# Kernel tuning notes

Measured on AMD Instinct MI355X. Metric: run time of the kernel, lower is better.

## Reference

```python
import jax, jax.numpy as jnp
import numpy as np

B, N, D, H, O = 4096, 128, 64, 256, 128  # batch, memory_size, memory_dim, controller_dim, output_size


def setup_inputs() -> dict:
    key = jax.random.key(0)
    ks = jax.random.split(key, 20)
    s = 0.05
    inp = {
        "x": jax.random.normal(ks[0], (B, O), jnp.float32),
        "memory": jax.random.normal(ks[1], (B, N, D), jnp.float32),
        "h": jax.random.normal(ks[2], (B, H), jnp.float32),
        "c": jax.random.normal(ks[3], (B, H), jnp.float32),
        # LSTMCell params (torch layout: gates ordered i, f, g, o; input = x||read_vec of width O+D)
        "W_ih": jax.random.normal(ks[4], (4 * H, O + D), jnp.float32) * s,
        "W_hh": jax.random.normal(ks[5], (4 * H, H), jnp.float32) * s,
        "b_ih": jax.random.normal(ks[6], (4 * H,), jnp.float32) * s,
        "b_hh": jax.random.normal(ks[7], (4 * H,), jnp.float32) * s,
        "W_read": jax.random.normal(ks[8], (N, H), jnp.float32) * s,
        "b_read": jax.random.normal(ks[9], (N,), jnp.float32) * s,
        "W_write": jax.random.normal(ks[10], (N, H), jnp.float32) * s,
        "b_write": jax.random.normal(ks[11], (N,), jnp.float32) * s,
        "W_erase": jax.random.normal(ks[12], (D, H), jnp.float32) * s,
        "b_erase": jax.random.normal(ks[13], (D,), jnp.float32) * s,
        "W_add": jax.random.normal(ks[14], (D, H), jnp.float32) * s,
        "b_add": jax.random.normal(ks[15], (D,), jnp.float32) * s,
        "W_out": jax.random.normal(ks[16], (O, H + D), jnp.float32) * s,
        "b_out": jax.random.normal(ks[17], (O,), jnp.float32) * s,
    }
    return inp


def reference(x, memory, h, c, W_ih, W_hh, b_ih, b_hh, W_read, b_read,
              W_write, b_write, W_erase, b_erase, W_add, b_add, W_out, b_out):
    # read: softmax attention over memory rows, addressed by previous hidden state
    read_w = jax.nn.softmax(h @ W_read.T + b_read, axis=-1)          # [B, N]
    read_vec = jnp.einsum("bn,bnd->bd", read_w, memory)               # [B, D]

    # LSTMCell step (torch gate order: i, f, g, o)
    ctrl_in = jnp.concatenate([x, read_vec], axis=-1)                 # [B, O+D]
    gates = ctrl_in @ W_ih.T + b_ih + h @ W_hh.T + b_hh               # [B, 4H]
    i, f, g, o = jnp.split(gates, 4, axis=-1)
    i, f, o = jax.nn.sigmoid(i), jax.nn.sigmoid(f), jax.nn.sigmoid(o)
    g = jnp.tanh(g)
    c_new = f * c + i * g
    h_new = o * jnp.tanh(c_new)

    # write: outer-product erase/add update
    write_w = jax.nn.softmax(h_new @ W_write.T + b_write, axis=-1)    # [B, N]
    erase = jax.nn.sigmoid(h_new @ W_erase.T + b_erase)               # [B, D]
    add = jnp.tanh(h_new @ W_add.T + b_add)                           # [B, D]
    ww = write_w[:, :, None]                                          # [B, N, 1]
    mem_new = memory * (1.0 - ww * erase[:, None, :]) + ww * add[:, None, :]

    out = jnp.concatenate([h_new, read_vec], axis=-1) @ W_out.T + b_out  # [B, O]
    return (out, mem_new, h_new, c_new)
```

## Files before the change

### kernel.cpp

```cpp
#include <hip/hip_runtime.h>
#include <math.h>


typedef __attribute__((ext_vector_type(8))) short bf16x8;
typedef __attribute__((ext_vector_type(4))) float f32x4;
typedef __attribute__((ext_vector_type(4))) unsigned short us4;

#define MFMA16(a, b, c) __builtin_amdgcn_mfma_f32_16x16x32_bf16(a, b, c, 0, 0, 0)
#define GLL16(gp, lp) __builtin_amdgcn_global_load_lds( \
    (const __attribute__((address_space(1))) void*)(gp), \
    (__attribute__((address_space(3))) void*)(lp), 16, 0, 0)
#define SW(row, s) ((s) ^ ((row) & 3))

__device__ __forceinline__ float sigf(float v) { return 1.f / (1.f + __expf(-v)); }

__device__ __forceinline__ unsigned short f2bf(float f) {
    unsigned u = __builtin_bit_cast(unsigned, f);
    u = (u + 0x7FFFu + ((u >> 16) & 1u)) >> 16;
    return (unsigned short)u;
}

__global__ __launch_bounds__(256) void kA_scores(
    const float* __restrict__ h, const float* __restrict__ Wr,
    const float* __restrict__ br, float* __restrict__ read_w)
{
    __shared__ unsigned short As[16 * 32];
    __shared__ unsigned short Bs[128 * 32];
    __shared__ float sc[16][128];

    int t = threadIdx.x;
    int wid = t >> 6, lane = t & 63;
    int cl = lane & 15, ks = lane >> 4;
    int b0 = blockIdx.x * 16;

    int aOff = cl * 32 + SW(cl, ks) * 8;
    int bOff[4];
#pragma unroll
    for (int f = 0; f < 4; ++f) {
        int br_ = (wid * 4 + f) * 16 + cl;
        bOff[f] = br_ * 32 + SW(br_, ks) * 8;
    }
    f32x4 acc[4] = {};
    for (int kc = 0; kc < 8; ++kc) {
        __syncthreads();
        {
            int row = t >> 4, k0 = (t & 15) * 2;
            float2 hv = *(const float2*)(h + (size_t)(b0 + row) * 256 + kc * 32 + k0);
            unsigned pk = (unsigned)f2bf(hv.x) | ((unsigned)f2bf(hv.y) << 16);
            *(unsigned*)(As + row * 32 + SW(row, k0 >> 3) * 8 + (k0 & 7)) = pk;
        }
        {
            int row = t >> 1, k0 = (t & 1) * 16;
            const float4* wp = (const float4*)(Wr + (size_t)row * 256 + kc * 32 + k0);
            float4 w0 = wp[0], w1 = wp[1], w2 = wp[2], w3 = wp[3];
            us4 p0 = { f2bf(w0.x), f2bf(w0.y), f2bf(w0.z), f2bf(w0.w) };
            us4 p1 = { f2bf(w1.x), f2bf(w1.y), f2bf(w1.z), f2bf(w1.w) };
            us4 p2 = { f2bf(w2.x), f2bf(w2.y), f2bf(w2.z), f2bf(w2.w) };
            us4 p3 = { f2bf(w3.x), f2bf(w3.y), f2bf(w3.z), f2bf(w3.w) };
            int g0 = k0 >> 3;
            unsigned short* basep = Bs + row * 32;
            *(us4*)(basep + SW(row, g0) * 8)         = p0;
            *(us4*)(basep + SW(row, g0) * 8 + 4)     = p1;
            *(us4*)(basep + SW(row, g0 + 1) * 8)     = p2;
            *(us4*)(basep + SW(row, g0 + 1) * 8 + 4) = p3;
        }
        __syncthreads();
        if (wid < 2) {
            bf16x8 a = *(const bf16x8*)(As + aOff);
#pragma unroll
            for (int f = 0; f < 4; ++f)
                acc[f] = MFMA16(a, *(const bf16x8*)(Bs + bOff[f]), acc[f]);
        }
    }
    if (wid < 2) {
#pragma unroll
        for (int f = 0; f < 4; ++f)
#pragma unroll
            for (int r = 0; r < 4; ++r)
                sc[ks * 4 + r][(wid * 4 + f) * 16 + cl] = acc[f][r];
    }
    __syncthreads();
    {
        int row = t >> 4, l = t & 15;
        float v[8];
#pragma unroll
        for (int j = 0; j < 8; ++j) v[j] = sc[row][l + 16 * j] + br[l + 16 * j];
        float m = v[0];
#pragma unroll
        for (int j = 1; j < 8; ++j) m = fmaxf(m, v[j]);
#pragma unroll
        for (int mk = 8; mk >= 1; mk >>= 1) m = fmaxf(m, __shfl_xor(m, mk));
        float s = 0.f;
#pragma unroll
        for (int j = 0; j < 8; ++j) { v[j] = __expf(v[j] - m); s += v[j]; }
#pragma unroll
        for (int mk = 8; mk >= 1; mk >>= 1) s += __shfl_xor(s, mk);
        float inv = 1.f / s;
#pragma unroll
        for (int j = 0; j < 8; ++j)
            read_w[(size_t)(b0 + row) * 128 + l + 16 * j] = v[j] * inv;
    }
}

__global__ __launch_bounds__(256) void k2_stream_pack(
    const float* __restrict__ mem, const float* __restrict__ read_w,
    const float* __restrict__ x, const float* __restrict__ h,
    const float* __restrict__ Wih, const float* __restrict__ Whh,
    const float* __restrict__ bih, const float* __restrict__ bhh,
    const float* __restrict__ Ww, const float* __restrict__ We,
    const float* __restrict__ Wa, const float* __restrict__ bw,
    const float* __restrict__ be, const float* __restrict__ ba,
    const float* __restrict__ Wo,
    unsigned short* __restrict__ Wg, unsigned short* __restrict__ Wh_b,
    unsigned short* __restrict__ Wo_b, float* __restrict__ bsum,
    float* __restrict__ bh_b, unsigned short* __restrict__ Ag,
    unsigned short* __restrict__ Aout)
{
    __shared__ float part[16][68];
    int t = threadIdx.x;
    int b = blockIdx.x;
    unsigned idx = b * 256 + t;

    if (idx < 458752) {
        int r = idx / 448, cc = idx - r * 448;
        float v = (cc < 192) ? Wih[(size_t)r * 192 + cc] : Whh[(size_t)r * 256 + (cc - 192)];
        Wg[idx] = f2bf(v);
    }
    if (idx < 65536) {
        int r = idx >> 8, cc = idx & 255;
        float v = (r < 128) ? Ww[(size_t)r * 256 + cc]
                : (r < 192) ? We[(size_t)(r - 128) * 256 + cc]
                            : Wa[(size_t)(r - 192) * 256 + cc];
        Wh_b[idx] = f2bf(v);
    }
    if (idx < 40960) Wo_b[idx] = f2bf(Wo[idx]);
    if (idx < 1024)  bsum[idx] = bih[idx] + bhh[idx];
    if (idx < 256)
        bh_b[idx] = (idx < 128) ? bw[idx] : (idx < 192 ? be[idx - 128] : ba[idx - 192]);

    if (t < 96) {
        int j = t;
        float4 v = (j < 32) ? ((const float4*)(x + (size_t)b * 128))[j]
                            : ((const float4*)(h + (size_t)b * 256))[j - 32];
        us4 o = { f2bf(v.x), f2bf(v.y), f2bf(v.z), f2bf(v.w) };
        int col = (j < 32) ? j * 4 : 192 + (j - 32) * 4;
        *(us4*)(Ag + (size_t)b * 448 + col) = o;
    }

    int np = t >> 4, d4 = t & 15;
    const float4* m4 = (const float4*)(mem + (size_t)b * 8192);
    float4 acc = make_float4(0.f, 0.f, 0.f, 0.f);
#pragma unroll
    for (int j = 0; j < 8; ++j) {
        int n = np + 16 * j;
        float w = read_w[(size_t)b * 128 + n];
        float4 mv = m4[t + 256 * j];
        acc.x += w * mv.x; acc.y += w * mv.y; acc.z += w * mv.z; acc.w += w * mv.w;
    }
    part[np][d4 * 4 + 0] = acc.x; part[np][d4 * 4 + 1] = acc.y;
    part[np][d4 * 4 + 2] = acc.z; part[np][d4 * 4 + 3] = acc.w;
    __syncthreads();
    if (t < 64) {
        float s = 0.f;
#pragma unroll
        for (int q = 0; q < 16; ++q) s += part[q][t];
        unsigned short bv = f2bf(s);
        Ag[(size_t)b * 448 + 128 + t] = bv;
        Aout[(size_t)b * 320 + 256 + t] = bv;
    }
}

__global__ __launch_bounds__(256) void kB_gates(
    const unsigned short* __restrict__ Ag, const unsigned short* __restrict__ Wg,
    const float* __restrict__ bsum, const float* __restrict__ c,
    float* __restrict__ h_new, float* __restrict__ c_new,
    unsigned short* __restrict__ Aout)
{
    __shared__ unsigned short As[32 * 32];
    __shared__ unsigned short Bs[256 * 32];
    int t = threadIdx.x;
    int wid = t >> 6, lane = t & 63;
    int cl = lane & 15, ks = lane >> 4;
    int b0 = blockIdx.x * 32;
    int u0 = blockIdx.y * 64;

    int arow = (t >> 2) & 31;
    const unsigned short* aSrc = Ag + (size_t)(b0 + arow) * 448 + SW(arow, t & 3) * 8;
    unsigned short* aDst = As + wid * 512;
    const unsigned short* bSrc[4];
    unsigned short* bDst[4];
#pragma unroll
    for (int j = 0; j < 4; ++j) {
        int rl = (j * 256 + t) >> 2;
        int g = rl >> 6, u = rl & 63;
        bSrc[j] = Wg + (size_t)(g * 256 + u0 + u) * 448 + SW(rl, t & 3) * 8;
        bDst[j] = Bs + (j * 256 + wid * 64) * 8;
    }

    int aOff[2];
#pragma unroll
    for (int rf = 0; rf < 2; ++rf) {
        int mr = rf * 16 + cl;
        aOff[rf] = mr * 32 + SW(mr, ks) * 8;
    }
    int bOff[4];
#pragma unroll
    for (int g = 0; g < 4; ++g) {
        int br_ = g * 64 + wid * 16 + cl;
        bOff[g] = br_ * 32 + SW(br_, ks) * 8;
    }

    f32x4 acc[2][4] = {};
    for (int kc = 0; kc < 14; ++kc) {
        __syncthreads();
        if (wid < 2) GLL16(aSrc, aDst);
        GLL16(bSrc[0], bDst[0]); GLL16(bSrc[1], bDst[1]);
        GLL16(bSrc[2], bDst[2]); GLL16(bSrc[3], bDst[3]);
        aSrc += 32;
#pragma unroll
        for (int j = 0; j < 4; ++j) bSrc[j] += 32;
        __syncthreads();
        bf16x8 a[2], b[4];
#pragma unroll
        for (int rf = 0; rf < 2; ++rf) a[rf] = *(const bf16x8*)(As + aOff[rf]);
#pragma unroll
        for (int g = 0; g < 4; ++g) b[g] = *(const bf16x8*)(Bs + bOff[g]);
#pragma unroll
        for (int rf = 0; rf < 2; ++rf)
#pragma unroll
            for (int g = 0; g < 4; ++g)
                acc[rf][g] = MFMA16(a[rf], b[g], acc[rf][g]);
    }

    int unit = u0 + wid * 16 + cl;
    float bi = bsum[unit], bf_ = bsum[256 + unit];
    float bg = bsum[512 + unit], bo_ = bsum[768 + unit];
#pragma unroll
    for (int rf = 0; rf < 2; ++rf) {
#pragma unroll
        for (int r = 0; r < 4; ++r) {
            int row = b0 + rf * 16 + ks * 4 + r;
            float iv = sigf(acc[rf][0][r] + bi);
            float fv = sigf(acc[rf][1][r] + bf_);
            float gv = tanhf(acc[rf][2][r] + bg);
            float ov = sigf(acc[rf][3][r] + bo_);
            float cv = fv * c[(size_t)row * 256 + unit] + iv * gv;
            float hv = ov * tanhf(cv);
            c_new[(size_t)row * 256 + unit] = cv;
            h_new[(size_t)row * 256 + unit] = hv;
            Aout[(size_t)row * 320 + unit] = f2bf(hv);
        }
    }
}

__global__ __launch_bounds__(256) void kC_heads_out(
    const unsigned short* __restrict__ Aout, const unsigned short* __restrict__ Wh_b,
    const unsigned short* __restrict__ Wo_b, const float* __restrict__ bh_b,
    const float* __restrict__ bo, float* __restrict__ write_w,
    float* __restrict__ erase, float* __restrict__ addv, float* __restrict__ outp)
{
    __shared__ unsigned short As[16 * 32];
    __shared__ unsigned short Bh[256 * 32];
    __shared__ unsigned short Bo[128 * 32];
    __shared__ float sc[16][256];

    int t = threadIdx.x;
    int wid = t >> 6, lane = t & 63;
    int cl = lane & 15, ks = lane >> 4;
    int b0 = blockIdx.x * 16;

    const unsigned short* aSrc = Aout + (size_t)(b0 + (lane >> 2)) * 320 + SW(lane >> 2, lane & 3) * 8;
    const unsigned short* bhSrc[4];
    unsigned short* bhDst[4];
#pragma unroll
    for (int j = 0; j < 4; ++j) {
        int rl = (j * 256 + t) >> 2;
        bhSrc[j] = Wh_b + (size_t)rl * 256 + SW(rl, t & 3) * 8;
        bhDst[j] = Bh + (j * 256 + wid * 64) * 8;
    }
    const unsigned short* boSrc[2];
    unsigned short* boDst[2];
#pragma unroll
    for (int j = 0; j < 2; ++j) {
        int rj = j * 64 + (t >> 2);
        boSrc[j] = Wo_b + (size_t)rj * 320 + SW(rj, t & 3) * 8;
        boDst[j] = Bo + j * 2048 + wid * 512;
    }

    int aOff = cl * 32 + SW(cl, ks) * 8;
    int bOffH[4], bOffO[2];
#pragma unroll
    for (int f = 0; f < 4; ++f) { int br_ = (wid * 4 + f) * 16 + cl; bOffH[f] = br_ * 32 + SW(br_, ks) * 8; }
#pragma unroll
    for (int f = 0; f < 2; ++f) { int br_ = (wid * 2 + f) * 16 + cl; bOffO[f] = br_ * 32 + SW(br_, ks) * 8; }

    f32x4 accH[4] = {};
    f32x4 accO[2] = {};
    for (int kc = 0; kc < 10; ++kc) {
        __syncthreads();
        if (t < 64) GLL16(aSrc, As);
        if (kc < 8) {
            GLL16(bhSrc[0], bhDst[0]); GLL16(bhSrc[1], bhDst[1]);
            GLL16(bhSrc[2], bhDst[2]); GLL16(bhSrc[3], bhDst[3]);
        }
        GLL16(boSrc[0], boDst[0]); GLL16(boSrc[1], boDst[1]);
        aSrc += 32;
#pragma unroll
        for (int j = 0; j < 4; ++j) bhSrc[j] += 32;
#pragma unroll
        for (int j = 0; j < 2; ++j) boSrc[j] += 32;
        __syncthreads();
        bf16x8 a = *(const bf16x8*)(As + aOff);
        if (kc < 8) {
#pragma unroll
            for (int f = 0; f < 4; ++f)
                accH[f] = MFMA16(a, *(const bf16x8*)(Bh + bOffH[f]), accH[f]);
        }
#pragma unroll
        for (int f = 0; f < 2; ++f)
            accO[f] = MFMA16(a, *(const bf16x8*)(Bo + bOffO[f]), accO[f]);
    }

#pragma unroll
    for (int f = 0; f < 4; ++f) {
        int col = (wid * 4 + f) * 16 + cl;
        float bb = bh_b[col];
#pragma unroll
        for (int r = 0; r < 4; ++r)
            sc[ks * 4 + r][col] = accH[f][r] + bb;
    }
#pragma unroll
    for (int f = 0; f < 2; ++f) {
        int col = (wid * 2 + f) * 16 + cl;
        float bb = bo[col];
#pragma unroll
        for (int r = 0; r < 4; ++r)
            outp[(size_t)(b0 + ks * 4 + r) * 128 + col] = accO[f][r] + bb;
    }
    __syncthreads();
    {
        int row = t >> 4, l = t & 15;
        float v[8];
#pragma unroll
        for (int j = 0; j < 8; ++j) v[j] = sc[row][l + 16 * j];
        float m = v[0];
#pragma unroll
        for (int j = 1; j < 8; ++j) m = fmaxf(m, v[j]);
#pragma unroll
        for (int mk = 8; mk >= 1; mk >>= 1) m = fmaxf(m, __shfl_xor(m, mk));
        float s = 0.f;
#pragma unroll
        for (int j = 0; j < 8; ++j) { v[j] = __expf(v[j] - m); s += v[j]; }
#pragma unroll
        for (int mk = 8; mk >= 1; mk >>= 1) s += __shfl_xor(s, mk);
        float inv = 1.f / s;
        int row_g = b0 + row;
#pragma unroll
        for (int j = 0; j < 8; ++j)
            write_w[(size_t)row_g * 128 + l + 16 * j] = v[j] * inv;
#pragma unroll
        for (int j = 0; j < 4; ++j)
            erase[(size_t)row_g * 64 + l + 16 * j] = sigf(sc[row][128 + l + 16 * j]);
#pragma unroll
        for (int j = 0; j < 4; ++j)
            addv[(size_t)row_g * 64 + l + 16 * j] = tanhf(sc[row][192 + l + 16 * j]);
    }
}

__global__ __launch_bounds__(256) void k5_mem_update(
    const float* __restrict__ mem, const float* __restrict__ write_w,
    const float* __restrict__ erase, const float* __restrict__ addv,
    float* __restrict__ mem_new)
{
    int t = threadIdx.x; int b = blockIdx.x;
    int np = t >> 4, d0 = (t & 15) * 4;
    const f32x4* m4 = (const f32x4*)(mem + (size_t)b * 8192);
    f32x4* o4 = (f32x4*)(mem_new + (size_t)b * 8192);
    f32x4 e4 = *(const f32x4*)(erase + (size_t)b * 64 + d0);
    f32x4 a4 = *(const f32x4*)(addv + (size_t)b * 64 + d0);
#pragma unroll
    for (int j = 0; j < 8; ++j) {
        int n = np + 16 * j;
        float w = write_w[(size_t)b * 128 + n];
        f32x4 m = m4[t + 256 * j];
        f32x4 r;
        r[0] = m[0] * (1.f - w * e4[0]) + w * a4[0];
        r[1] = m[1] * (1.f - w * e4[1]) + w * a4[1];
        r[2] = m[2] * (1.f - w * e4[2]) + w * a4[2];
        r[3] = m[3] * (1.f - w * e4[3]) + w * a4[3];
        __builtin_nontemporal_store(r, &o4[t + 256 * j]);
    }
}

extern "C" void kernel_launch(void* const* d_in, const int* in_sizes, int n_in,
                              void* d_out, int out_size, void* d_ws, size_t ws_size,
                              hipStream_t stream)
{
    const float* x    = (const float*)d_in[0];
    const float* mem  = (const float*)d_in[1];
    const float* h    = (const float*)d_in[2];
    const float* c    = (const float*)d_in[3];
    const float* Wih  = (const float*)d_in[4];
    const float* Whh  = (const float*)d_in[5];
    const float* bih  = (const float*)d_in[6];
    const float* bhh  = (const float*)d_in[7];
    const float* Wr   = (const float*)d_in[8];
    const float* br   = (const float*)d_in[9];
    const float* Ww   = (const float*)d_in[10];
    const float* bw   = (const float*)d_in[11];
    const float* We   = (const float*)d_in[12];
    const float* be   = (const float*)d_in[13];
    const float* Wa   = (const float*)d_in[14];
    const float* ba   = (const float*)d_in[15];
    const float* Wo   = (const float*)d_in[16];
    const float* bo   = (const float*)d_in[17];

    float* out     = (float*)d_out;
    float* mem_new = out + 524288;
    float* h_new   = out + 34078720;
    float* c_new   = out + 35127296;

    float* ws      = (float*)d_ws;
    float* read_w  = ws;
    float* write_w = ws + 524288;
    float* erase   = ws + 1048576;
    float* addv    = ws + 1310720;
    float* bsum    = ws + 1572864;
    float* bh_b    = ws + 1573888;
    unsigned short* ub   = (unsigned short*)(ws + 1574144);
    unsigned short* Ag   = ub;
    unsigned short* Aout = ub + 1835008;
    unsigned short* Wg   = ub + 3145728;
    unsigned short* Wh_b = ub + 3604480;
    unsigned short* Wo_b = ub + 3670016;

    kA_scores<<<256, 256, 0, stream>>>(h, Wr, br, read_w);
    k2_stream_pack<<<4096, 256, 0, stream>>>(mem, read_w, x, h, Wih, Whh, bih, bhh,
                                             Ww, We, Wa, bw, be, ba, Wo,
                                             Wg, Wh_b, Wo_b, bsum, bh_b, Ag, Aout);
    kB_gates<<<dim3(128, 4), 256, 0, stream>>>(Ag, Wg, bsum, c, h_new, c_new, Aout);
    kC_heads_out<<<256, 256, 0, stream>>>(Aout, Wh_b, Wo_b, bh_b, bo,
                                          write_w, erase, addv, out);
    k5_mem_update<<<4096, 256, 0, stream>>>(mem, write_w, erase, addv, mem_new);
}
```

Before: 105.2 us.

## Widen gates K-tile to 64 and halve heads kernel batch tile

The gates GEMM now stages a K-chunk of 64 per iteration with an 8-way XOR swizzle, so the K loop runs 7 times instead of 14. That halves the barrier and load-issue overhead per MFMA. The heads/output kernel now handles 8 batch rows per block instead of 16 and launches twice as many blocks. It preloads the whole bf16 activation row into LDS up front, and MFMA rows 8-15 are duplicated and discarded. This trades redundant MFMA work and extra weight reloads per block for more parallelism and fewer global loads inside the loop.

```diff
diff --git a/kernel.cpp b/kernel.cpp
--- a/kernel.cpp
+++ b/kernel.cpp
@@ -18,6 +18,10 @@
     unsigned u = __builtin_bit_cast(unsigned, f);
     u = (u + 0x7FFFu + ((u >> 16) & 1u)) >> 16;
     return (unsigned short)u;
+}
+
+__device__ __forceinline__ int swA8(int r, int c) {
+    return r * 320 + (c & ~31) + ((((c >> 3) & 3) ^ (r & 3)) << 3) + (c & 7);
 }
 
 __global__ __launch_bounds__(256) void kA_scores(
@@ -176,60 +180,68 @@
     float* __restrict__ h_new, float* __restrict__ c_new,
     unsigned short* __restrict__ Aout)
 {
-    __shared__ unsigned short As[32 * 32];
-    __shared__ unsigned short Bs[256 * 32];
+    __shared__ unsigned short As[32 * 64];
+    __shared__ unsigned short Bs[256 * 64];
     int t = threadIdx.x;
     int wid = t >> 6, lane = t & 63;
     int cl = lane & 15, ks = lane >> 4;
     int b0 = blockIdx.x * 32;
     int u0 = blockIdx.y * 64;
 
-    int arow = (t >> 2) & 31;
-    const unsigned short* aSrc = Ag + (size_t)(b0 + arow) * 448 + SW(arow, t & 3) * 8;
-    unsigned short* aDst = As + wid * 512;
-    const unsigned short* bSrc[4];
-    unsigned short* bDst[4];
-#pragma unroll
-    for (int j = 0; j < 4; ++j) {
-        int rl = (j * 256 + t) >> 2;
+    int arow = t >> 3, aseg = t & 7;
+    const unsigned short* aSrc = Ag + (size_t)(b0 + arow) * 448 + ((aseg ^ (arow & 7)) * 8);
+    unsigned short* aDst = As + t * 8;
+    const unsigned short* bSrc[8];
+    unsigned short* bDst[8];
+#pragma unroll
+    for (int j = 0; j < 8; ++j) {
+        int i = j * 256 + t;
+        int rl = i >> 3, seg = i & 7;
         int g = rl >> 6, u = rl & 63;
-        bSrc[j] = Wg + (size_t)(g * 256 + u0 + u) * 448 + SW(rl, t & 3) * 8;
-        bDst[j] = Bs + (j * 256 + wid * 64) * 8;
-    }
-
-    int aOff[2];
-#pragma unroll
-    for (int rf = 0; rf < 2; ++rf) {
-        int mr = rf * 16 + cl;
-        aOff[rf] = mr * 32 + SW(mr, ks) * 8;
-    }
-    int bOff[4];
-#pragma unroll
-    for (int g = 0; g < 4; ++g) {
-        int br_ = g * 64 + wid * 16 + cl;
-        bOff[g] = br_ * 32 + SW(br_, ks) * 8;
-    }
+        bSrc[j] = Wg + (size_t)(g * 256 + u0 + u) * 448 + ((seg ^ (rl & 7)) * 8);
+        bDst[j] = Bs + i * 8;
+    }
+
+    int aOff[2][2];
+#pragma unroll
+    for (int rf = 0; rf < 2; ++rf)
+#pragma unroll
+        for (int kk = 0; kk < 2; ++kk) {
+            int mr = rf * 16 + cl;
+            aOff[rf][kk] = mr * 64 + (((kk * 4 + ks) ^ (cl & 7)) * 8);
+        }
+    int bOff[4][2];
+#pragma unroll
+    for (int g = 0; g < 4; ++g)
+#pragma unroll
+        for (int kk = 0; kk < 2; ++kk) {
+            int br_ = g * 64 + wid * 16 + cl;
+            bOff[g][kk] = br_ * 64 + (((kk * 4 + ks) ^ (cl & 7)) * 8);
+        }
 
     f32x4 acc[2][4] = {};
-    for (int kc = 0; kc < 14; ++kc) {
-        __syncthreads();
-        if (wid < 2) GLL16(aSrc, aDst);
-        GLL16(bSrc[0], bDst[0]); GLL16(bSrc[1], bDst[1]);
-        GLL16(bSrc[2], bDst[2]); GLL16(bSrc[3], bDst[3]);
-        aSrc += 32;
-#pragma unroll
-        for (int j = 0; j < 4; ++j) bSrc[j] += 32;
-        __syncthreads();
-        bf16x8 a[2], b[4];
-#pragma unroll
-        for (int rf = 0; rf < 2; ++rf) a[rf] = *(const bf16x8*)(As + aOff[rf]);
-#pragma unroll
-        for (int g = 0; g < 4; ++g) b[g] = *(const bf16x8*)(Bs + bOff[g]);
-#pragma unroll
-        for (int rf = 0; rf < 2; ++rf)
-#pragma unroll
-            for (int g = 0; g < 4; ++g)
-                acc[rf][g] = MFMA16(a[rf], b[g], acc[rf][g]);
+    for (int kc = 0; kc < 7; ++kc) {
+        __syncthreads();
+        GLL16(aSrc, aDst);
+#pragma unroll
+        for (int j = 0; j < 8; ++j) GLL16(bSrc[j], bDst[j]);
+        aSrc += 64;
+#pragma unroll
+        for (int j = 0; j < 8; ++j) bSrc[j] += 64;
+        __syncthreads();
+#pragma unroll
+        for (int kk = 0; kk < 2; ++kk) {
+            bf16x8 a[2], b[4];
+#pragma unroll
+            for (int rf = 0; rf < 2; ++rf) a[rf] = *(const bf16x8*)(As + aOff[rf][kk]);
+#pragma unroll
+            for (int g = 0; g < 4; ++g) b[g] = *(const bf16x8*)(Bs + bOff[g][kk]);
+#pragma unroll
+            for (int rf = 0; rf < 2; ++rf)
+#pragma unroll
+                for (int g = 0; g < 4; ++g)
+                    acc[rf][g] = MFMA16(a[rf], b[g], acc[rf][g]);
+        }
     }
 
     int unit = u0 + wid * 16 + cl;
@@ -259,17 +271,22 @@
     const float* __restrict__ bo, float* __restrict__ write_w,
     float* __restrict__ erase, float* __restrict__ addv, float* __restrict__ outp)
 {
-    __shared__ unsigned short As[16 * 32];
+    __shared__ unsigned short As8[8 * 320];
     __shared__ unsigned short Bh[256 * 32];
     __shared__ unsigned short Bo[128 * 32];
-    __shared__ float sc[16][256];
+    __shared__ float sc8[8][256];
 
     int t = threadIdx.x;
     int wid = t >> 6, lane = t & 63;
     int cl = lane & 15, ks = lane >> 4;
-    int b0 = blockIdx.x * 16;
-
-    const unsigned short* aSrc = Aout + (size_t)(b0 + (lane >> 2)) * 320 + SW(lane >> 2, lane & 3) * 8;
+    int r0 = blockIdx.x * 8;
+
+    for (int i = t; i < 640; i += 256) {
+        int row = i / 80, c4 = (i - row * 80) * 4;
+        us4 v = *(const us4*)(Aout + (size_t)(r0 + row) * 320 + c4);
+        *(us4*)(As8 + swA8(row, c4)) = v;
+    }
+
     const unsigned short* bhSrc[4];
     unsigned short* bhDst[4];
 #pragma unroll
@@ -287,62 +304,61 @@
         boDst[j] = Bo + j * 2048 + wid * 512;
     }
 
-    int aOff = cl * 32 + SW(cl, ks) * 8;
     int bOffH[4], bOffO[2];
 #pragma unroll
-    for (int f = 0; f < 4; ++f) { int br_ = (wid * 4 + f) * 16 + cl; bOffH[f] = br_ * 32 + SW(br_, ks) * 8; }
-#pragma unroll
-    for (int f = 0; f < 2; ++f) { int br_ = (wid * 2 + f) * 16 + cl; bOffO[f] = br_ * 32 + SW(br_, ks) * 8; }
+    for (int j = 0; j < 4; ++j) { int br_ = (wid + 4 * j) * 16 + cl; bOffH[j] = br_ * 32 + SW(br_, ks) * 8; }
+#pragma unroll
+    for (int j = 0; j < 2; ++j) { int br_ = (wid + 4 * j) * 16 + cl; bOffO[j] = br_ * 32 + SW(br_, ks) * 8; }
 
     f32x4 accH[4] = {};
     f32x4 accO[2] = {};
     for (int kc = 0; kc < 10; ++kc) {
         __syncthreads();
-        if (t < 64) GLL16(aSrc, As);
         if (kc < 8) {
             GLL16(bhSrc[0], bhDst[0]); GLL16(bhSrc[1], bhDst[1]);
             GLL16(bhSrc[2], bhDst[2]); GLL16(bhSrc[3], bhDst[3]);
+#pragma unroll
+            for (int j = 0; j < 4; ++j) bhSrc[j] += 32;
         }
         GLL16(boSrc[0], boDst[0]); GLL16(boSrc[1], boDst[1]);
-        aSrc += 32;
-#pragma unroll
-        for (int j = 0; j < 4; ++j) bhSrc[j] += 32;
 #pragma unroll
         for (int j = 0; j < 2; ++j) boSrc[j] += 32;
         __syncthreads();
-        bf16x8 a = *(const bf16x8*)(As + aOff);
+        bf16x8 a = *(const bf16x8*)(As8 + swA8(cl & 7, kc * 32 + ks * 8));
         if (kc < 8) {
 #pragma unroll
-            for (int f = 0; f < 4; ++f)
-                accH[f] = MFMA16(a, *(const bf16x8*)(Bh + bOffH[f]), accH[f]);
-        }
-#pragma unroll
-        for (int f = 0; f < 2; ++f)
-            accO[f] = MFMA16(a, *(const bf16x8*)(Bo + bOffO[f]), accO[f]);
-    }
-
-#pragma unroll
-    for (int f = 0; f < 4; ++f) {
-        int col = (wid * 4 + f) * 16 + cl;
-        float bb = bh_b[col];
-#pragma unroll
-        for (int r = 0; r < 4; ++r)
-            sc[ks * 4 + r][col] = accH[f][r] + bb;
-    }
-#pragma unroll
-    for (int f = 0; f < 2; ++f) {
-        int col = (wid * 2 + f) * 16 + cl;
-        float bb = bo[col];
-#pragma unroll
-        for (int r = 0; r < 4; ++r)
-            outp[(size_t)(b0 + ks * 4 + r) * 128 + col] = accO[f][r] + bb;
+            for (int j = 0; j < 4; ++j)
+                accH[j] = MFMA16(a, *(const bf16x8*)(Bh + bOffH[j]), accH[j]);
+        }
+#pragma unroll
+        for (int j = 0; j < 2; ++j)
+            accO[j] = MFMA16(a, *(const bf16x8*)(Bo + bOffO[j]), accO[j]);
+    }
+
+    if (ks < 2) {
+#pragma unroll
+        for (int j = 0; j < 4; ++j) {
+            int col = (wid + 4 * j) * 16 + cl;
+            float bb = bh_b[col];
+#pragma unroll
+            for (int r = 0; r < 4; ++r) sc8[ks * 4 + r][col] = accH[j][r] + bb;
+        }
+#pragma unroll
+        for (int j = 0; j < 2; ++j) {
+            int ocol = (wid + 4 * j) * 16 + cl;
+            float bb = bo[ocol];
+#pragma unroll
+            for (int r = 0; r < 4; ++r)
+                outp[(size_t)(r0 + ks * 4 + r) * 128 + ocol] = accO[j][r] + bb;
+        }
     }
     __syncthreads();
-    {
+
+    if (t < 128) {
         int row = t >> 4, l = t & 15;
         float v[8];
 #pragma unroll
-        for (int j = 0; j < 8; ++j) v[j] = sc[row][l + 16 * j];
+        for (int j = 0; j < 8; ++j) v[j] = sc8[row][l + 16 * j];
         float m = v[0];
 #pragma unroll
         for (int j = 1; j < 8; ++j) m = fmaxf(m, v[j]);
@@ -354,16 +370,16 @@
 #pragma unroll
         for (int mk = 8; mk >= 1; mk >>= 1) s += __shfl_xor(s, mk);
         float inv = 1.f / s;
-        int row_g = b0 + row;
+        int row_g = r0 + row;
 #pragma unroll
         for (int j = 0; j < 8; ++j)
             write_w[(size_t)row_g * 128 + l + 16 * j] = v[j] * inv;
 #pragma unroll
         for (int j = 0; j < 4; ++j)
-            erase[(size_t)row_g * 64 + l + 16 * j] = sigf(sc[row][128 + l + 16 * j]);
+            erase[(size_t)row_g * 64 + l + 16 * j] = sigf(sc8[row][128 + l + 16 * j]);
 #pragma unroll
         for (int j = 0; j < 4; ++j)
-            addv[(size_t)row_g * 64 + l + 16 * j] = tanhf(sc[row][192 + l + 16 * j]);
+            addv[(size_t)row_g * 64 + l + 16 * j] = tanhf(sc8[row][192 + l + 16 * j]);
     }
 }
 
@@ -439,7 +455,7 @@
                                              Ww, We, Wa, bw, be, ba, Wo,
                                              Wg, Wh_b, Wo_b, bsum, bh_b, Ag, Aout);
     kB_gates<<<dim3(128, 4), 256, 0, stream>>>(Ag, Wg, bsum, c, h_new, c_new, Aout);
-    kC_heads_out<<<256, 256, 0, stream>>>(Aout, Wh_b, Wo_b, bh_b, bo,
+    kC_heads_out<<<512, 256, 0, stream>>>(Aout, Wh_b, Wo_b, bh_b, bo,
                                           write_w, erase, addv, out);
     k5_mem_update<<<4096, 256, 0, stream>>>(mem, write_w, erase, addv, mem_new);
 }
```

Measured after the change: 103.3 us, median of 2. About the same (-1.8%).
